# Performance work log

Measured on AMD Instinct MI355X. Metric: run time of the kernel, lower is better.

The kernel has to match this reference:

```python
import jax, jax.numpy as jnp
import numpy as np

B, T, DIM = 2, 2048, 1024
N_HEADS, HEAD_DIM, WINDOW = 16, 64, 512
EPS = 0.01


def _rmsnorm(x, gamma, eps):
    # x: [B, T, H*D] float32; normalize over last dim
    rms = jnp.sqrt(jnp.mean(jnp.square(x), axis=-1, keepdims=True) + eps)
    return x / rms * gamma


def setup_inputs() -> dict:
    key = jax.random.key(0)
    ks = jax.random.split(key, 5)
    s = 1.0 / np.sqrt(DIM)
    return {
        "x": jax.random.normal(ks[0], (B, T, DIM), jnp.float32),
        "wq": jax.random.normal(ks[1], (N_HEADS * HEAD_DIM, DIM), jnp.float32) * s,
        "wk": jax.random.normal(ks[2], (N_HEADS * HEAD_DIM, DIM), jnp.float32) * s,
        "wv": jax.random.normal(ks[3], (N_HEADS * HEAD_DIM, DIM), jnp.float32) * s,
        "wo": jax.random.normal(ks[4], (DIM, N_HEADS * HEAD_DIM), jnp.float32) * s,
        "q_gamma": jnp.ones((N_HEADS * HEAD_DIM,), jnp.float32),
        "k_gamma": jnp.ones((N_HEADS * HEAD_DIM,), jnp.float32),
    }


def reference(x, wq, wk, wv, wo, q_gamma, k_gamma):
    Bx, Tx, _ = x.shape
    H, D = N_HEADS, HEAD_DIM
    # projections (Linear with weight [out,in]): [B,T,H*D]
    q = x @ wq.T
    k = x @ wk.T
    v = (x @ wv.T).reshape(Bx, Tx, H, D).transpose(0, 2, 1, 3)  # [B,H,T,D]
    # QK RMSNorm over the flattened H*D dimension (float32 math)
    q = _rmsnorm(q, q_gamma, 1e-6).reshape(Bx, Tx, H, D).transpose(0, 2, 1, 3)
    k = _rmsnorm(k, k_gamma, 1e-6).reshape(Bx, Tx, H, D).transpose(0, 2, 1, 3)
    scale = 1.0 / np.sqrt(D)
    scores = jnp.einsum("bhqd,bhkd->bhqk", q, k) * scale  # [B,H,T,T]
    # ALiBi bias: slopes[h] * (j - i)
    slopes = jnp.asarray([2.0 ** (-8.0 / H * (h + 1)) for h in range(H)], jnp.float32)
    pos = jnp.arange(Tx)
    dist = (pos[None, :] - pos[:, None]).astype(jnp.float32)  # [T,T], dist[i,j]=j-i
    scores = scores + slopes[None, :, None, None] * dist[None, None]
    # causal (j>i) OR beyond sliding window (i-j > window_size)
    j_minus_i = pos[None, :] - pos[:, None]
    mask = (j_minus_i > 0) | (j_minus_i < -WINDOW)
    scores = jnp.where(mask[None, None], -1e9, scores)
    attn = jax.nn.softmax(scores, axis=-1)
    out = jnp.einsum("bhqk,bhkd->bhqd", attn, v)  # [B,H,T,D]
    out = out.transpose(0, 2, 1, 3).reshape(Bx, Tx, H * D)
    return out @ wo.T
```

## Files before the change

### kernel.cpp

```cpp
#include <hip/hip_runtime.h>
#include <stdint.h>

typedef unsigned short u16;
typedef __bf16 bf16x8 __attribute__((ext_vector_type(8)));
typedef float f32x4 __attribute__((ext_vector_type(4)));

#define MFMA16(a, b, c) __builtin_amdgcn_mfma_f32_16x16x32_bf16((a), (b), (c), 0, 0, 0)

__device__ __forceinline__ u16 f2bf(float f) {
  union { float f; uint32_t u; } v; v.f = f;
  uint32_t r = v.u + 0x7fffu + ((v.u >> 16) & 1u);
  return (u16)(r >> 16);
}
__device__ __forceinline__ float bf2f(u16 h) {
  union { uint32_t u; float f; } v; v.u = ((uint32_t)h) << 16;
  return v.f;
}
__device__ __forceinline__ void gload_lds16(const void* g, void* l) {
  __builtin_amdgcn_global_load_lds(
      (const __attribute__((address_space(1))) uint32_t*)(uintptr_t)g,
      (__attribute__((address_space(3))) uint32_t*)(uintptr_t)l, 16, 0, 0);
}
__device__ __forceinline__ uint32_t cvt_pk_bf16(float a, float b) {
  uint32_t r;
  asm("v_cvt_pk_bf16_f32 %0, %1, %2" : "=v"(r) : "v"(a), "v"(b));
  return r;
}

__global__ void k_cvt_all(const float* __restrict__ x, const float* __restrict__ wq,
                          const float* __restrict__ wk, const float* __restrict__ wv,
                          const float* __restrict__ wo, u16* __restrict__ xb,
                          u16* __restrict__ wqb, u16* __restrict__ wkb, u16* __restrict__ wvb,
                          u16* __restrict__ wob) {
  const int i = blockIdx.x * 256 + threadIdx.x;
  const float* src; u16* dst; int off;
  if (i < 1048576)      { src = x;  dst = xb;  off = i; }
  else if (i < 1310720) { src = wq; dst = wqb; off = i - 1048576; }
  else if (i < 1572864) { src = wk; dst = wkb; off = i - 1310720; }
  else if (i < 1835008) { src = wv; dst = wvb; off = i - 1572864; }
  else                  { src = wo; dst = wob; off = i - 1835008; }
  const float4 v = ((const float4*)src)[off];
  u16 o[4] = { f2bf(v.x), f2bf(v.y), f2bf(v.z), f2bf(v.w) };
  *(uint2*)(dst + 4 * (size_t)off) = *(const uint2*)o;
}

template <bool BF16_OUT>
__device__ __forceinline__ void gemm_core(const u16* __restrict__ A, const u16* __restrict__ Bw,
                                          void* __restrict__ C, int tm, int tn) {
  constexpr int K = 1024, N = 1024, NT = K / 32;
  __shared__ __align__(16) u16 As[2][128 * 32];
  __shared__ __align__(16) u16 Bs[2][128 * 32];
  const int tid = threadIdx.x, l = tid & 63, w = tid >> 6;
  const int wm = (w >> 1) * 64, wn = (w & 1) * 64;
  const int lo = l & 15, hi8 = (l >> 4) * 8;
  f32x4 acc[4][4] = {};

  const int srow = l >> 2, scol = (l & 3) * 8;
  const int c0 = w * 2, c1 = w * 2 + 1;
  const u16* Ag0 = A + (size_t)(tm + c0 * 16 + srow) * K + scol;
  const u16* Ag1 = A + (size_t)(tm + c1 * 16 + srow) * K + scol;
  const u16* Bg0 = Bw + (size_t)(tn + c0 * 16 + srow) * K + scol;
  const u16* Bg1 = Bw + (size_t)(tn + c1 * 16 + srow) * K + scol;

#define STAGE_G(t, buf)                           \
  {                                               \
    const int kt_ = (t) * 32;                     \
    gload_lds16(Ag0 + kt_, &As[(buf)][c0 * 512]); \
    gload_lds16(Ag1 + kt_, &As[(buf)][c1 * 512]); \
    gload_lds16(Bg0 + kt_, &Bs[(buf)][c0 * 512]); \
    gload_lds16(Bg1 + kt_, &Bs[(buf)][c1 * 512]); \
  }

  STAGE_G(0, 0);
  STAGE_G(1, 1);

  for (int t = 0; t < NT; ++t) {
    const int cur = t & 1;
    if (t + 1 < NT) {
      asm volatile("s_waitcnt vmcnt(4)");
    } else {
      asm volatile("s_waitcnt vmcnt(0)");
    }
    __builtin_amdgcn_s_barrier();
    __builtin_amdgcn_sched_barrier(0);

    bf16x8 af[4], bfr[4];
#pragma unroll
    for (int m = 0; m < 4; ++m) af[m] = *(const bf16x8*)&As[cur][(wm + m * 16 + lo) * 32 + hi8];
#pragma unroll
    for (int n = 0; n < 4; ++n) bfr[n] = *(const bf16x8*)&Bs[cur][(wn + n * 16 + lo) * 32 + hi8];
#pragma unroll
    for (int m = 0; m < 4; ++m)
#pragma unroll
      for (int n = 0; n < 4; ++n) acc[m][n] = MFMA16(af[m], bfr[n], acc[m][n]);

    __builtin_amdgcn_sched_barrier(0);
    __builtin_amdgcn_s_barrier();
    __builtin_amdgcn_sched_barrier(0);
    if (t + 2 < NT) STAGE_G(t + 2, cur);
  }
#undef STAGE_G

  const int r0 = (l >> 4) * 4;
#pragma unroll
  for (int m = 0; m < 4; ++m)
#pragma unroll
    for (int n = 0; n < 4; ++n)
#pragma unroll
      for (int r = 0; r < 4; ++r) {
        const size_t idx = (size_t)(tm + wm + m * 16 + r0 + r) * N + (tn + wn + n * 16 + lo);
        if (BF16_OUT) ((u16*)C)[idx] = f2bf(acc[m][n][r]);
        else ((float*)C)[idx] = acc[m][n][r];
      }
}

__global__ __launch_bounds__(256, 3) void k_gemm_qkv(
    const u16* __restrict__ X, const u16* __restrict__ Wq, const u16* __restrict__ Wk,
    const u16* __restrict__ Wv, u16* __restrict__ Q, u16* __restrict__ Kt, u16* __restrict__ V) {
  const int n = blockIdx.x + (blockIdx.y << 3) + (blockIdx.z << 8);
  const int wid = (n & 7) * 96 + (n >> 3);
  const int bz = wid >> 8, rem = wid & 255, by = rem >> 3, bx = rem & 7;
  const u16* B = bz == 0 ? Wq : bz == 1 ? Wk : Wv;
  u16* C = bz == 0 ? Q : bz == 1 ? Kt : V;
  gemm_core<true>(X, B, C, by * 128, bx * 128);
}
__global__ __launch_bounds__(256, 3) void k_gemm_out(const u16* __restrict__ Ao,
                                                     const u16* __restrict__ Wo,
                                                     float* __restrict__ C) {
  const int n = blockIdx.x + (blockIdx.y << 3);
  const int wid = (n & 7) * 32 + (n >> 3);
  const int by = wid >> 3, bx = wid & 7;
  gemm_core<false>(Ao, Wo, C, by * 128, bx * 128);
}

__global__ __launch_bounds__(256) void k_rmsnorm(u16* __restrict__ Q, u16* __restrict__ Kt,
                                                 const float* __restrict__ qg,
                                                 const float* __restrict__ kg) {
  const int row = blockIdx.x;
  u16* base = (row < 4096) ? (Q + (size_t)row * 1024) : (Kt + (size_t)(row - 4096) * 1024);
  const float* g = (row < 4096) ? qg : kg;
  const int tid = threadIdx.x;
  ushort4 v = ((const ushort4*)base)[tid];
  float f0 = bf2f(v.x), f1 = bf2f(v.y), f2 = bf2f(v.z), f3 = bf2f(v.w);
  float ss = f0 * f0 + f1 * f1 + f2 * f2 + f3 * f3;
#pragma unroll
  for (int off = 32; off >= 1; off >>= 1) ss += __shfl_xor(ss, off, 64);
  __shared__ float wsum[4];
  if ((tid & 63) == 0) wsum[tid >> 6] = ss;
  __syncthreads();
  ss = wsum[0] + wsum[1] + wsum[2] + wsum[3];
  const float rinv = rsqrtf(ss * (1.0f / 1024.0f) + 1e-6f);
  const float4 gv = ((const float4*)g)[tid];
  v.x = f2bf(f0 * rinv * gv.x);
  v.y = f2bf(f1 * rinv * gv.y);
  v.z = f2bf(f2 * rinv * gv.z);
  v.w = f2bf(f3 * rinv * gv.w);
  ((ushort4*)base)[tid] = v;
}

__global__ __launch_bounds__(512, 4) void k_attn(const u16* __restrict__ Q,
                                                 const u16* __restrict__ Kt,
                                                 const u16* __restrict__ V,
                                                 u16* __restrict__ O) {
  constexpr int T = 2048, HD = 1024, WIN = 512;
  const int nlin = blockIdx.x + (blockIdx.y << 4) + (blockIdx.z << 8);
  const int wid = (nlin & 7) * 64 + (nlin >> 3);
  const int qb = (wid & 15) * 128, h = (wid >> 4) & 15, b = wid >> 8;
  const int tid = threadIdx.x, l = tid & 63, w = tid >> 6;
  const int lo = l & 15, hi = l >> 4;
  const int qw = qb + w * 16;
  const int qg = qw + lo;

  __shared__ __align__(16) u16 Ks[2][64 * 64];
  __shared__ __align__(16) u16 Vt[2][64 * 72];

  const size_t bT = (size_t)b * T;

  bf16x8 qf[2];
  {
    const u16* Qr = Q + (bT + qw + lo) * HD + h * 64 + hi * 8;
    qf[0] = *(const bf16x8*)(Qr);
    qf[1] = *(const bf16x8*)(Qr + 32);
  }

  const int srow = tid >> 3;
  const int kcol = 8 * ((tid & 7) ^ (srow & 7));
  const int vkv = 2 * (l & 31) + (l >> 5);
  const int vd0 = w * 8;
  const u16* Kg0 = Kt + bT * HD + h * 64;
  const u16* Vg0 = V + bT * HD + h * 64;

  float m_r = -1e30f, l_r = 0.f;
  f32x4 o_acc[4] = {};

  const float L2E = 1.4426950408889634f;
  const float scaleL = 0.125f * L2E;
  const float slopeL = exp2f(-0.5f * (float)(h + 1)) * L2E;
  float cn[4], cr[4];
#pragma unroll
  for (int n = 0; n < 4; ++n) cn[n] = slopeL * (float)(n * 16);
#pragma unroll
  for (int r = 0; r < 4; ++r) cr[r] = slopeL * (float)r;

  const int kvs = (qb >= WIN) ? (qb - WIN) : 0;
  const int nt = (qb + 128 - kvs) >> 6;

  {
    const uint4 pkt = *(const uint4*)(Vg0 + (size_t)(kvs + vkv) * HD + vd0);
    gload_lds16(Kg0 + (size_t)(kvs + srow) * HD + kcol, &Ks[0][tid * 8]);
    const u16* e = (const u16*)&pkt;
#pragma unroll
    for (int j = 0; j < 8; ++j) Vt[0][(vd0 + j) * 72 + vkv] = e[j];
  }
  asm volatile("s_waitcnt vmcnt(0)");
  asm volatile("s_waitcnt lgkmcnt(0)");
  __builtin_amdgcn_s_barrier();
  __builtin_amdgcn_sched_barrier(0);

  for (int t = 0; t < nt; ++t) {
    const int kv0 = kvs + t * 64, cur = t & 1;
    const bool pf_next = (t + 1 < nt);
    uint4 vnext;
    if (pf_next) {
      vnext = *(const uint4*)(Vg0 + (size_t)(kv0 + 64 + vkv) * HD + vd0);
      gload_lds16(Kg0 + (size_t)(kv0 + 64 + srow) * HD + kcol, &Ks[cur ^ 1][tid * 8]);
    }

    const bool active = (kv0 <= qw + 15) && (kv0 + 63 + WIN >= qw);
    if (active) {
      f32x4 st[4];
      __builtin_amdgcn_s_setprio(1);
#pragma unroll
      for (int n = 0; n < 4; ++n) {
        f32x4 z = {0.f, 0.f, 0.f, 0.f};
        const int row = n * 16 + lo;
        const int swz = (row & 7) << 4;
#pragma unroll
        for (int kk = 0; kk < 2; ++kk) {
          const bf16x8 kf =
              *(const bf16x8*)((const char*)Ks[cur] + row * 128 + ((kk * 64 + hi * 16) ^ swz));
          z = MFMA16(kf, qf[kk], z);
        }
        st[n] = z;
      }
      __builtin_amdgcn_s_setprio(0);

      const int ddb = kv0 + hi * 4 - qg;
      const float bb = slopeL * (float)ddb;
      float bn[4];
#pragma unroll
      for (int n = 0; n < 4; ++n) bn[n] = bb + cn[n];
      const bool interior = (kv0 + 63 <= qw) && (qw + 15 - kv0 <= WIN);
      if (interior) {
#pragma unroll
        for (int n = 0; n < 4; ++n)
#pragma unroll
          for (int r = 0; r < 4; ++r) st[n][r] = st[n][r] * scaleL + (bn[n] + cr[r]);
      } else {
#pragma unroll
        for (int n = 0; n < 4; ++n)
#pragma unroll
          for (int r = 0; r < 4; ++r) {
            const int dd = ddb + n * 16 + r;
            const float s_ = st[n][r] * scaleL + (bn[n] + cr[r]);
            st[n][r] = (dd > 0 || dd < -WIN) ? -1e30f : s_;
          }
      }

      float mx = -1e30f;
#pragma unroll
      for (int n = 0; n < 4; ++n) {
        const float a = fmaxf(st[n][0], st[n][1]), c = fmaxf(st[n][2], st[n][3]);
        mx = fmaxf(mx, fmaxf(a, c));
      }
      mx = fmaxf(mx, __shfl_xor(mx, 16, 64));
      mx = fmaxf(mx, __shfl_xor(mx, 32, 64));
      const float mn = fmaxf(m_r, mx);
      const float alpha = exp2f(m_r - mn);
      m_r = mn;

      float rs = 0.f;
#pragma unroll
      for (int n = 0; n < 4; ++n)
#pragma unroll
        for (int r = 0; r < 4; ++r) {
          const float p = exp2f(st[n][r] - mn);
          st[n][r] = p;
          rs += p;
        }
      rs += __shfl_xor(rs, 16, 64);
      rs += __shfl_xor(rs, 32, 64);
      l_r = l_r * alpha + rs;
#pragma unroll
      for (int nd = 0; nd < 4; ++nd)
#pragma unroll
        for (int r = 0; r < 4; ++r) o_acc[nd][r] *= alpha;

      uint32_t pk[4][2];
#pragma unroll
      for (int n = 0; n < 4; ++n)
#pragma unroll
        for (int d = 0; d < 2; ++d) pk[n][d] = cvt_pk_bf16(st[n][2 * d], st[n][2 * d + 1]);

      uint32_t pfr[2][4];
#pragma unroll
      for (int kk = 0; kk < 2; ++kk)
#pragma unroll
        for (int d = 0; d < 2; ++d) {
          auto s1 = __builtin_amdgcn_permlane32_swap(pk[kk * 2][d], pk[kk * 2 + 1][d], false, false);
          auto s2 = __builtin_amdgcn_permlane16_swap(s1[0], s1[1], false, false);
          pfr[kk][d] = s2[0];
          pfr[kk][2 + d] = s2[1];
        }

      __builtin_amdgcn_s_setprio(1);
#pragma unroll
      for (int kk = 0; kk < 2; ++kk) {
        union { uint32_t u[4]; bf16x8 v; } pu;
#pragma unroll
        for (int d2 = 0; d2 < 4; ++d2) pu.u[d2] = pfr[kk][d2];
        const bf16x8 pv = pu.v;
#pragma unroll
        for (int nd = 0; nd < 4; ++nd) {
          const bf16x8 vf = *(const bf16x8*)&Vt[cur][(nd * 16 + lo) * 72 + kk * 32 + hi * 8];
          o_acc[nd] = MFMA16(vf, pv, o_acc[nd]);
        }
      }
      __builtin_amdgcn_s_setprio(0);
    }

    if (pf_next) {
      const u16* e = (const u16*)&vnext;
#pragma unroll
      for (int j = 0; j < 8; ++j) Vt[cur ^ 1][(vd0 + j) * 72 + vkv] = e[j];
    }
    __builtin_amdgcn_sched_barrier(0);
    asm volatile("s_waitcnt lgkmcnt(0)");
    asm volatile("s_waitcnt vmcnt(0)");
    __builtin_amdgcn_s_barrier();
    __builtin_amdgcn_sched_barrier(0);
  }

  const float inv = 1.f / l_r;
  u16* Og = O + (bT + qw + lo) * HD + h * 64;
#pragma unroll
  for (int nd = 0; nd < 4; ++nd) {
    uint2 pack;
    pack.x = cvt_pk_bf16(o_acc[nd][0] * inv, o_acc[nd][1] * inv);
    pack.y = cvt_pk_bf16(o_acc[nd][2] * inv, o_acc[nd][3] * inv);
    *(uint2*)(Og + nd * 16 + hi * 4) = pack;
  }
}

extern "C" void kernel_launch(void* const* d_in, const int* in_sizes, int n_in,
                              void* d_out, int out_size, void* d_ws, size_t ws_size,
                              hipStream_t stream) {
  const float* x = (const float*)d_in[0];
  const float* wq = (const float*)d_in[1];
  const float* wk = (const float*)d_in[2];
  const float* wv = (const float*)d_in[3];
  const float* wo = (const float*)d_in[4];
  const float* qg = (const float*)d_in[5];
  const float* kg = (const float*)d_in[6];
  float* out = (float*)d_out;

  char* ws = (char*)d_ws;
  const size_t MB = (size_t)1 << 20;
  u16* xb  = (u16*)(ws + 0 * MB);
  u16* wqb = (u16*)(ws + 8 * MB);
  u16* wkb = (u16*)(ws + 10 * MB);
  u16* wvb = (u16*)(ws + 12 * MB);
  u16* wob = (u16*)(ws + 14 * MB);
  u16* qb  = (u16*)(ws + 16 * MB);
  u16* kb  = (u16*)(ws + 24 * MB);
  u16* vb  = (u16*)(ws + 32 * MB);
  u16* ab  = xb;

  k_cvt_all<<<8192, 256, 0, stream>>>(x, wq, wk, wv, wo, xb, wqb, wkb, wvb, wob);
  k_gemm_qkv<<<dim3(8, 32, 3), 256, 0, stream>>>(xb, wqb, wkb, wvb, qb, kb, vb);
  k_rmsnorm<<<8192, 256, 0, stream>>>(qb, kb, qg, kg);
  k_attn<<<dim3(16, 16, 2), 512, 0, stream>>>(qb, kb, vb, ab);
  k_gemm_out<<<dim3(8, 32, 1), 256, 0, stream>>>(ab, wob, out);
}
```

Baseline: 102.2 us.

## Shrink output GEMM tile to 128x64 and add lazy softmax rescaling

The output projection GEMM now uses a 128x64 tile with a 512-block grid, raising block count and occupancy (launch bound 4) so the 256-CU device is better filled. In attention, the online softmax skips the running-max update and accumulator rescale when the whole wave's new max exceeds the old one by at most 8 (log2 units), saving exp and multiply work on most tiles. The lazy rescale allows unnormalised probabilities up to 2^8 before bf16 packing, which slightly changes precision. The smaller GEMM tile lowers the reuse of the A operand.

```diff
diff --git a/kernel.cpp b/kernel.cpp
--- a/kernel.cpp
+++ b/kernel.cpp
@@ -44,16 +44,18 @@
   *(uint2*)(dst + 4 * (size_t)off) = *(const uint2*)o;
 }
 
-template <bool BF16_OUT>
+template <bool BF16_OUT, int BN>
 __device__ __forceinline__ void gemm_core(const u16* __restrict__ A, const u16* __restrict__ Bw,
                                           void* __restrict__ C, int tm, int tn) {
   constexpr int K = 1024, N = 1024, NT = K / 32;
+  constexpr int MF = (BN == 128) ? 4 : 2;
   __shared__ __align__(16) u16 As[2][128 * 32];
-  __shared__ __align__(16) u16 Bs[2][128 * 32];
+  __shared__ __align__(16) u16 Bs[2][BN * 32];
   const int tid = threadIdx.x, l = tid & 63, w = tid >> 6;
-  const int wm = (w >> 1) * 64, wn = (w & 1) * 64;
+  const int wm = (BN == 128) ? (w >> 1) * 64 : w * 32;
+  const int wn = (BN == 128) ? (w & 1) * 64 : 0;
   const int lo = l & 15, hi8 = (l >> 4) * 8;
-  f32x4 acc[4][4] = {};
+  f32x4 acc[MF][4] = {};
 
   const int srow = l >> 2, scol = (l & 3) * 8;
   const int c0 = w * 2, c1 = w * 2 + 1;
@@ -61,14 +63,19 @@
   const u16* Ag1 = A + (size_t)(tm + c1 * 16 + srow) * K + scol;
   const u16* Bg0 = Bw + (size_t)(tn + c0 * 16 + srow) * K + scol;
   const u16* Bg1 = Bw + (size_t)(tn + c1 * 16 + srow) * K + scol;
-
-#define STAGE_G(t, buf)                           \
-  {                                               \
-    const int kt_ = (t) * 32;                     \
-    gload_lds16(Ag0 + kt_, &As[(buf)][c0 * 512]); \
-    gload_lds16(Ag1 + kt_, &As[(buf)][c1 * 512]); \
-    gload_lds16(Bg0 + kt_, &Bs[(buf)][c0 * 512]); \
-    gload_lds16(Bg1 + kt_, &Bs[(buf)][c1 * 512]); \
+  const u16* BgB = Bw + (size_t)(tn + (tid >> 2)) * K + (tid & 3) * 8;
+
+#define STAGE_G(t, buf)                                  \
+  {                                                      \
+    const int kt_ = (t) * 32;                            \
+    gload_lds16(Ag0 + kt_, &As[(buf)][c0 * 512]);        \
+    gload_lds16(Ag1 + kt_, &As[(buf)][c1 * 512]);        \
+    if constexpr (BN == 128) {                           \
+      gload_lds16(Bg0 + kt_, &Bs[(buf)][c0 * 512]);      \
+      gload_lds16(Bg1 + kt_, &Bs[(buf)][c1 * 512]);      \
+    } else {                                             \
+      gload_lds16(BgB + kt_, &Bs[(buf)][tid * 8]);       \
+    }                                                    \
   }
 
   STAGE_G(0, 0);
@@ -77,20 +84,21 @@
   for (int t = 0; t < NT; ++t) {
     const int cur = t & 1;
     if (t + 1 < NT) {
-      asm volatile("s_waitcnt vmcnt(4)");
+      if constexpr (BN == 128) asm volatile("s_waitcnt vmcnt(4)");
+      else asm volatile("s_waitcnt vmcnt(3)");
     } else {
       asm volatile("s_waitcnt vmcnt(0)");
     }
     __builtin_amdgcn_s_barrier();
     __builtin_amdgcn_sched_barrier(0);
 
-    bf16x8 af[4], bfr[4];
-#pragma unroll
-    for (int m = 0; m < 4; ++m) af[m] = *(const bf16x8*)&As[cur][(wm + m * 16 + lo) * 32 + hi8];
+    bf16x8 af[MF], bfr[4];
+#pragma unroll
+    for (int m = 0; m < MF; ++m) af[m] = *(const bf16x8*)&As[cur][(wm + m * 16 + lo) * 32 + hi8];
 #pragma unroll
     for (int n = 0; n < 4; ++n) bfr[n] = *(const bf16x8*)&Bs[cur][(wn + n * 16 + lo) * 32 + hi8];
 #pragma unroll
-    for (int m = 0; m < 4; ++m)
+    for (int m = 0; m < MF; ++m)
 #pragma unroll
       for (int n = 0; n < 4; ++n) acc[m][n] = MFMA16(af[m], bfr[n], acc[m][n]);
 
@@ -103,7 +111,7 @@
 
   const int r0 = (l >> 4) * 4;
 #pragma unroll
-  for (int m = 0; m < 4; ++m)
+  for (int m = 0; m < MF; ++m)
 #pragma unroll
     for (int n = 0; n < 4; ++n)
 #pragma unroll
@@ -122,15 +130,15 @@
   const int bz = wid >> 8, rem = wid & 255, by = rem >> 3, bx = rem & 7;
   const u16* B = bz == 0 ? Wq : bz == 1 ? Wk : Wv;
   u16* C = bz == 0 ? Q : bz == 1 ? Kt : V;
-  gemm_core<true>(X, B, C, by * 128, bx * 128);
-}
-__global__ __launch_bounds__(256, 3) void k_gemm_out(const u16* __restrict__ Ao,
+  gemm_core<true, 128>(X, B, C, by * 128, bx * 128);
+}
+__global__ __launch_bounds__(256, 4) void k_gemm_out(const u16* __restrict__ Ao,
                                                      const u16* __restrict__ Wo,
                                                      float* __restrict__ C) {
-  const int n = blockIdx.x + (blockIdx.y << 3);
-  const int wid = (n & 7) * 32 + (n >> 3);
-  const int by = wid >> 3, bx = wid & 7;
-  gemm_core<false>(Ao, Wo, C, by * 128, bx * 128);
+  const int n = blockIdx.x + (blockIdx.y << 4);
+  const int wid = (n & 7) * 64 + (n >> 3);
+  const int by = wid >> 4, bx = wid & 15;
+  gemm_core<false, 64>(Ao, Wo, C, by * 128, bx * 64);
 }
 
 __global__ __launch_bounds__(256) void k_rmsnorm(u16* __restrict__ Q, u16* __restrict__ Kt,
@@ -275,26 +283,40 @@
       }
       mx = fmaxf(mx, __shfl_xor(mx, 16, 64));
       mx = fmaxf(mx, __shfl_xor(mx, 32, 64));
-      const float mn = fmaxf(m_r, mx);
-      const float alpha = exp2f(m_r - mn);
-      m_r = mn;
 
       float rs = 0.f;
-#pragma unroll
-      for (int n = 0; n < 4; ++n)
-#pragma unroll
-        for (int r = 0; r < 4; ++r) {
-          const float p = exp2f(st[n][r] - mn);
-          st[n][r] = p;
-          rs += p;
-        }
-      rs += __shfl_xor(rs, 16, 64);
-      rs += __shfl_xor(rs, 32, 64);
-      l_r = l_r * alpha + rs;
-#pragma unroll
-      for (int nd = 0; nd < 4; ++nd)
-#pragma unroll
-        for (int r = 0; r < 4; ++r) o_acc[nd][r] *= alpha;
+      if (__all(mx - m_r <= 8.0f)) {
+#pragma unroll
+        for (int n = 0; n < 4; ++n)
+#pragma unroll
+          for (int r = 0; r < 4; ++r) {
+            const float p = exp2f(st[n][r] - m_r);
+            st[n][r] = p;
+            rs += p;
+          }
+        rs += __shfl_xor(rs, 16, 64);
+        rs += __shfl_xor(rs, 32, 64);
+        l_r += rs;
+      } else {
+        const float mn = fmaxf(m_r, mx);
+        const float alpha = exp2f(m_r - mn);
+        m_r = mn;
+#pragma unroll
+        for (int n = 0; n < 4; ++n)
+#pragma unroll
+          for (int r = 0; r < 4; ++r) {
+            const float p = exp2f(st[n][r] - mn);
+            st[n][r] = p;
+            rs += p;
+          }
+        rs += __shfl_xor(rs, 16, 64);
+        rs += __shfl_xor(rs, 32, 64);
+        l_r = l_r * alpha + rs;
+#pragma unroll
+        for (int nd = 0; nd < 4; ++nd)
+#pragma unroll
+          for (int r = 0; r < 4; ++r) o_acc[nd][r] *= alpha;
+      }
 
       uint32_t pk[4][2];
 #pragma unroll
@@ -380,5 +402,5 @@
   k_gemm_qkv<<<dim3(8, 32, 3), 256, 0, stream>>>(xb, wqb, wkb, wvb, qb, kb, vb);
   k_rmsnorm<<<8192, 256, 0, stream>>>(qb, kb, qg, kg);
   k_attn<<<dim3(16, 16, 2), 512, 0, stream>>>(qb, kb, vb, ab);
-  k_gemm_out<<<dim3(8, 32, 1), 256, 0, stream>>>(ab, wob, out);
-}
+  k_gemm_out<<<dim3(16, 32), 256, 0, stream>>>(ab, wob, out);
+}
```

New measurement: 101.1 us. Within noise of the previous version (-1.1%).
